# Kernel optimization log

Measured on AMD Instinct MI355X. Metric: run time of the kernel, lower is better.

Reference implementation:

```python
import jax, jax.numpy as jnp
import numpy as np

B = 262144
IN = 256
HID = 128
OUT = 15
C = 15  # num_cameras


def setup_inputs() -> dict:
    key = jax.random.key(0)
    k_x, k_c, k_w1, k_b1, k_w2, k_b2 = jax.random.split(key, 6)
    x = jax.random.normal(k_x, (B, IN), dtype=jnp.float32)
    cam = jax.random.randint(k_c, (B,), 0, C)
    # per-camera 2-layer MLP params (Linear->ReLU->Dropout(eval)->Linear)
    W1 = jax.random.normal(k_w1, (C, IN, HID), dtype=jnp.float32) / np.sqrt(IN)
    b1 = jax.random.normal(k_b1, (C, HID), dtype=jnp.float32) * 0.01
    W2 = jax.random.normal(k_w2, (C, HID, OUT), dtype=jnp.float32) / np.sqrt(HID)
    b2 = jax.random.normal(k_b2, (C, OUT), dtype=jnp.float32) * 0.01
    return {"input": x, "cam": cam, "W1": W1, "b1": b1, "W2": W2, "b2": b2}


def reference(input, cam, W1, b1, W2, b2):
    # Per-sample camera-id dispatch to one of C small MLPs, vectorized:
    # run each camera's MLP on the full batch (C is small/fixed) and select
    # each sample's output by its camera id. Dropout is identity (eval mode).
    out = jnp.zeros((input.shape[0], OUT), dtype=input.dtype)
    for c in range(C):
        h = jax.nn.relu(input @ W1[c] + b1[c])      # [B, HID]
        logits = h @ W2[c] + b2[c]                  # [B, OUT]
        out = jnp.where((cam == c)[:, None], logits, out)
    return out
```

## Files before the change

kernel.cpp:

```cpp
#include <hip/hip_runtime.h>
#include <hip/hip_bf16.h>

#define BB    262144
#define INF   256
#define HIDF  128
#define OUTF  15
#define NCAM  15
#define TM    128
#define MAXTILES (BB/TM + NCAM)

typedef __attribute__((ext_vector_type(8))) short          bf16x8;
typedef __attribute__((ext_vector_type(4))) float          floatx4;
typedef __attribute__((ext_vector_type(4))) int            intx4;
typedef __attribute__((ext_vector_type(4))) unsigned int   uintx4;
typedef __attribute__((ext_vector_type(8))) unsigned short ushortx8;

__device__ __forceinline__ unsigned short f2bf1(float a){
  unsigned int u = __builtin_bit_cast(unsigned int, a);
  u += 0x7fffu + ((u >> 16) & 1u);
  return (unsigned short)(u >> 16);
}
__device__ __forceinline__ unsigned int f2bf2(float a, float b){
  return (unsigned int)f2bf1(a) | ((unsigned int)f2bf1(b) << 16);
}

__global__ void k_prephist(const float* __restrict__ W1, const float* __restrict__ W2,
                           const int* __restrict__ cam,
                           unsigned short* __restrict__ W1p, unsigned short* __restrict__ W2p,
                           int* __restrict__ counts){
  int bid = blockIdx.x, tid = threadIdx.x;
  if (bid < 240){
    int t = bid * 256 + tid;
    int l  = t & 63;
    int kf = (t >> 6) & 7;
    int nf = (t >> 9) & 7;
    int c  = t >> 12;
    int col = nf*16 + (l & 15);
    int k0  = kf*32 + (l >> 4)*8;
    ushortx8 v;
    #pragma unroll
    for (int j = 0; j < 8; ++j)
      v[j] = f2bf1(W1[((size_t)c*INF + k0 + j)*HIDF + col]);
    *reinterpret_cast<ushortx8*>(W1p + (size_t)t*8) = v;
  } else if (bid < 255){
    int c  = bid - 240;
    int l  = tid & 63;
    int kf = tid >> 6;
    int col = l & 15;
    int k0  = kf*32 + (l >> 4)*8;
    ushortx8 v;
    #pragma unroll
    for (int j = 0; j < 8; ++j){
      float f = (col < OUTF) ? W2[((size_t)c*HIDF + k0 + j)*OUTF + col] : 0.0f;
      v[j] = f2bf1(f);
    }
    *reinterpret_cast<ushortx8*>(W2p + ((size_t)(c*4 + kf)*64 + l)*8) = v;
  } else if (bid >= 256){
    __shared__ int lc[NCAM];
    if (tid < NCAM) lc[tid] = 0;
    __syncthreads();
    intx4 v = *reinterpret_cast<const intx4*>(cam + (size_t)((bid-256)*256 + tid)*4);
    atomicAdd(&lc[v[0]], 1); atomicAdd(&lc[v[1]], 1);
    atomicAdd(&lc[v[2]], 1); atomicAdd(&lc[v[3]], 1);
    __syncthreads();
    if (tid < NCAM && lc[tid]) atomicAdd(&counts[tid], lc[tid]);
  }
}

__global__ void k_scatter(const int* __restrict__ cam, const int* __restrict__ counts,
                          int* __restrict__ scatterOfs, int* __restrict__ idx){
  __shared__ int lc[NCAM];
  __shared__ int loff[NCAM];
  __shared__ int base[NCAM];
  int t = threadIdx.x;
  if (t < NCAM) lc[t] = 0;
  __syncthreads();
  int start = blockIdx.x * 4096;
  int camr[16], lpos[16];
  #pragma unroll
  for (int j = 0; j < 16; ++j){
    int i = start + j*256 + t;
    camr[j] = cam[i];
    lpos[j] = atomicAdd(&lc[camr[j]], 1);
  }
  __syncthreads();
  if (t == 0){
    int s = 0;
    #pragma unroll
    for (int c = 0; c < NCAM; ++c){ loff[c] = s; s += counts[c]; }
  }
  __syncthreads();
  if (t < NCAM) base[t] = loff[t] + atomicAdd(&scatterOfs[t], lc[t]);
  __syncthreads();
  #pragma unroll
  for (int j = 0; j < 16; ++j)
    idx[base[camr[j]] + lpos[j]] = start + j*256 + t;
}

__global__ __launch_bounds__(256, 2) void k_mlp(
    const float* __restrict__ x, const int* __restrict__ idx,
    const int* __restrict__ counts,
    const unsigned short* __restrict__ W1p, const unsigned short* __restrict__ W2p,
    const float* __restrict__ b1, const float* __restrict__ b2,
    float* __restrict__ out)
{
  __shared__ __align__(16) char smem[65536];

  int bid = blockIdx.x;
  intx4 q0 = *reinterpret_cast<const intx4*>(counts);
  intx4 q1 = *reinterpret_cast<const intx4*>(counts + 4);
  intx4 q2 = *reinterpret_cast<const intx4*>(counts + 8);
  intx4 q3 = *reinterpret_cast<const intx4*>(counts + 12);
  int cnt[16] = {q0[0],q0[1],q0[2],q0[3], q1[0],q1[1],q1[2],q1[3],
                 q2[0],q2[1],q2[2],q2[3], q3[0],q3[1],q3[2],q3[3]};
  int c = -1, segStart = 0, rowStart = 0, rows = 0;
  {
    int cum = 0, rcum = 0;
    #pragma unroll
    for (int cc = 0; cc < NCAM; ++cc){
      int n  = cnt[cc];
      int nt = (n + TM - 1) >> 7;
      if (c < 0 && bid < cum + nt){
        c = cc;
        rowStart = (bid - cum) * TM;
        segStart = rcum;
        rows = n - rowStart; if (rows > TM) rows = TM;
      }
      cum += nt; rcum += n;
    }
  }
  if (c < 0) return;

  int t = threadIdx.x;
  int wave = t >> 6, lane = t & 63;
  int wr  = wave * 32, l15 = lane & 15, lk = lane >> 4;
  const int* idxBase = idx + segStart + rowStart;

  const char* srcp[4];
  {
    int sr = lane >> 3, su = lane & 7;
    int woff = (su ^ sr) * 16;
    #pragma unroll
    for (int i = 0; i < 4; ++i){
      int row = wr + i*8 + sr;
      int rc = (row < rows) ? row : (rows - 1);
      srcp[i] = reinterpret_cast<const char*>(x) + (size_t)idxBase[rc]*1024 + woff;
    }
  }

  const unsigned short* bbase = W1p + (size_t)c*32768 + lane*8;

#define STAGE(qq) { \
    char* db = smem + ((qq)&3)*16384 + wave*4096; \
    _Pragma("unroll") \
    for (int i = 0; i < 4; ++i){ \
      __builtin_amdgcn_global_load_lds( \
        (const __attribute__((address_space(1))) unsigned int*)(srcp[i] + (qq)*128), \
        (__attribute__((address_space(3))) unsigned int*)(db + i*1024), \
        16, 0, 0); \
    } }

  floatx4 acc[2][8];
  #pragma unroll
  for (int i = 0; i < 2; ++i)
    #pragma unroll
    for (int j = 0; j < 8; ++j) acc[i][j] = (floatx4)0.0f;

  bf16x8 bfr[2][8];
  #pragma unroll
  for (int nf = 0; nf < 8; ++nf)
    bfr[0][nf] = *reinterpret_cast<const bf16x8*>(bbase + nf*4096);
  __builtin_amdgcn_sched_barrier(0);
  STAGE(0); STAGE(1); STAGE(2);
  __builtin_amdgcn_sched_barrier(0);

  int swz8 = l15 & 7;

  #pragma unroll
  for (int kf = 0; kf < 8; ++kf){
    if (kf < 7){
      #pragma unroll
      for (int nf = 0; nf < 8; ++nf)
        bfr[(kf+1)&1][nf] = *reinterpret_cast<const bf16x8*>(bbase + nf*4096 + (kf+1)*512);
    }
    __builtin_amdgcn_sched_barrier(0);
    if (kf < 5) STAGE(kf+3);
    __builtin_amdgcn_sched_barrier(0);
    if (kf == 0)      asm volatile("s_waitcnt vmcnt(20)" ::: "memory");
    else if (kf <= 4) asm volatile("s_waitcnt vmcnt(16)" ::: "memory");
    else if (kf == 5) asm volatile("s_waitcnt vmcnt(12)" ::: "memory");
    else if (kf == 6) asm volatile("s_waitcnt vmcnt(8)"  ::: "memory");
    else              asm volatile("s_waitcnt vmcnt(0)"  ::: "memory");
    __builtin_amdgcn_sched_barrier(0);

    bf16x8 af[2];
    #pragma unroll
    for (int mf = 0; mf < 2; ++mf){
      int rl = mf*16 + l15;
      const char* rb = smem + (kf&3)*16384 + wave*4096 + rl*128;
      floatx4 f0 = *reinterpret_cast<const floatx4*>(rb + (((2*lk)   ^ swz8) * 16));
      floatx4 f1 = *reinterpret_cast<const floatx4*>(rb + (((2*lk+1) ^ swz8) * 16));
      uintx4 u;
      u[0] = f2bf2(f0[0], f0[1]); u[1] = f2bf2(f0[2], f0[3]);
      u[2] = f2bf2(f1[0], f1[1]); u[3] = f2bf2(f1[2], f1[3]);
      af[mf] = __builtin_bit_cast(bf16x8, u);
    }
    #pragma unroll
    for (int nf = 0; nf < 8; ++nf)
      acc[0][nf] = __builtin_amdgcn_mfma_f32_16x16x32_bf16(af[0], bfr[kf&1][nf], acc[0][nf], 0, 0, 0);
    #pragma unroll
    for (int nf = 0; nf < 8; ++nf)
      acc[1][nf] = __builtin_amdgcn_mfma_f32_16x16x32_bf16(af[1], bfr[kf&1][nf], acc[1][nf], 0, 0, 0);
  }

  #pragma unroll
  for (int nf = 0; nf < 8; ++nf){
    int col = nf*16 + l15;
    float bias = b1[c*HIDF + col];
    #pragma unroll
    for (int mf = 0; mf < 2; ++mf){
      #pragma unroll
      for (int j = 0; j < 4; ++j){
        int rl = mf*16 + lk*4 + j;
        float h = fmaxf(acc[mf][nf][j] + bias, 0.0f);
        int off = (rl>>4)*16384 + wave*4096 + (rl&15)*256 + ((col*2) ^ ((rl&7)<<4));
        *reinterpret_cast<unsigned short*>(smem + off) = f2bf1(h);
      }
    }
  }

  floatx4 acc2[2];
  acc2[0] = (floatx4)0.0f; acc2[1] = (floatx4)0.0f;
  const unsigned short* wb = W2p + (size_t)c*2048 + lane*8;
  #pragma unroll
  for (int kf = 0; kf < 4; ++kf){
    bf16x8 wv = *reinterpret_cast<const bf16x8*>(wb + kf*512);
    #pragma unroll
    for (int mf = 0; mf < 2; ++mf){
      int rl = mf*16 + l15;
      int off = (rl>>4)*16384 + wave*4096 + (rl&15)*256 + ((kf*64 + lk*16) ^ ((rl&7)<<4));
      bf16x8 av = *reinterpret_cast<const bf16x8*>(smem + off);
      acc2[mf] = __builtin_amdgcn_mfma_f32_16x16x32_bf16(av, wv, acc2[mf], 0, 0, 0);
    }
  }

  int col = l15;
  if (col < OUTF){
    float bias2 = b2[c*OUTF + col];
    #pragma unroll
    for (int mf = 0; mf < 2; ++mf){
      #pragma unroll
      for (int j = 0; j < 4; ++j){
        int r = wr + mf*16 + lk*4 + j;
        if (r < rows)
          out[(size_t)idxBase[r]*OUTF + col] = acc2[mf][j] + bias2;
      }
    }
  }
#undef STAGE
}

extern "C" void kernel_launch(void* const* d_in, const int* in_sizes, int n_in,
                              void* d_out, int out_size, void* d_ws, size_t ws_size,
                              hipStream_t stream) {
  const float* x  = (const float*)d_in[0];
  const int*   cam= (const int*)d_in[1];
  const float* W1 = (const float*)d_in[2];
  const float* b1 = (const float*)d_in[3];
  const float* W2 = (const float*)d_in[4];
  const float* b2 = (const float*)d_in[5];
  float* out = (float*)d_out;

  char* ws = (char*)d_ws;
  int* counts     = (int*)(ws);
  int* scatterOfs = (int*)(ws + 64);
  int* idx        = (int*)(ws + 256);
  unsigned short* W1p = (unsigned short*)(ws + 256 + (size_t)BB*4);
  unsigned short* W2p = W1p + (size_t)NCAM*8*8*64*8;

  (void)hipMemsetAsync(counts, 0, 128, stream);
  hipLaunchKernelGGL(k_prephist, dim3(512),     dim3(256), 0, stream, W1, W2, cam, W1p, W2p, counts);
  hipLaunchKernelGGL(k_scatter,  dim3(BB/4096), dim3(256), 0, stream, cam, counts, scatterOfs, idx);
  hipLaunchKernelGGL(k_mlp,      dim3(MAXTILES),dim3(256), 0, stream,
                     x, idx, counts, W1p, W2p, b1, b2, out);
}
```

Before: 93.49 us.

## Load gathered rows through registers, convert to bf16 once, stage bf16 in LDS

Replaces the 4-stage async global_load_lds pipeline of fp32 x tiles with register loads. Each wave gathers its 32 rows by shuffling row indices, converts them to bf16 with the packed v_cvt_pk_bf16_f32 instruction, and writes the full 32x256 bf16 tile into a swizzled per-wave LDS region before the MFMA loop. This removes the repeated fp32-to-bf16 conversion inside the K loop and halves the LDS footprint for A. The cost is that load/compute overlap across K steps is lost, and register pressure rises from holding 16 float4 staging values.

```diff
diff --git a/kernel.cpp b/kernel.cpp
--- a/kernel.cpp
+++ b/kernel.cpp
@@ -12,7 +12,7 @@
 typedef __attribute__((ext_vector_type(8))) short          bf16x8;
 typedef __attribute__((ext_vector_type(4))) float          floatx4;
 typedef __attribute__((ext_vector_type(4))) int            intx4;
-typedef __attribute__((ext_vector_type(4))) unsigned int   uintx4;
+typedef __attribute__((ext_vector_type(2))) unsigned int   uintx2;
 typedef __attribute__((ext_vector_type(8))) unsigned short ushortx8;
 
 __device__ __forceinline__ unsigned short f2bf1(float a){
@@ -20,8 +20,10 @@
   u += 0x7fffu + ((u >> 16) & 1u);
   return (unsigned short)(u >> 16);
 }
-__device__ __forceinline__ unsigned int f2bf2(float a, float b){
-  return (unsigned int)f2bf1(a) | ((unsigned int)f2bf1(b) << 16);
+__device__ __forceinline__ unsigned int cvtpk(float a, float b){
+  unsigned int r;
+  asm("v_cvt_pk_bf16_f32 %0, %1, %2" : "=v"(r) : "v"(a), "v"(b));
+  return r;
 }
 
 __global__ void k_prephist(const float* __restrict__ W1, const float* __restrict__ W2,
@@ -133,48 +135,54 @@
 
   int t = threadIdx.x;
   int wave = t >> 6, lane = t & 63;
-  int wr  = wave * 32, l15 = lane & 15, lk = lane >> 4;
+  int wr = wave * 32, l15 = lane & 15, lk = lane >> 4;
   const int* idxBase = idx + segStart + rowStart;
 
-  const char* srcp[4];
-  {
-    int sr = lane >> 3, su = lane & 7;
-    int woff = (su ^ sr) * 16;
-    #pragma unroll
-    for (int i = 0; i < 4; ++i){
-      int row = wr + i*8 + sr;
-      int rc = (row < rows) ? row : (rows - 1);
-      srcp[i] = reinterpret_cast<const char*>(x) + (size_t)idxBase[rc]*1024 + woff;
-    }
-  }
+  int rr = wr + (lane & 31);
+  int gl = idxBase[(rr < rows) ? rr : (rows - 1)];
+
+  char* Aw = smem + wave*16384;
+
+  floatx4 lv0[8], lv1[8];
+
+  auto LOADB = [&](int b, floatx4 (&d)[8]){
+    #pragma unroll
+    for (int i = 0; i < 8; ++i){
+      int g = __shfl(gl, b*8 + i);
+      d[i] = *reinterpret_cast<const floatx4*>(x + (size_t)g*INF + lane*4);
+    }
+  };
+  auto WRITEB = [&](int b, floatx4 (&d)[8]){
+    #pragma unroll
+    for (int i = 0; i < 8; ++i){
+      int rl = b*8 + i;
+      uintx2 u;
+      u[0] = cvtpk(d[i][0], d[i][1]);
+      u[1] = cvtpk(d[i][2], d[i][3]);
+      *reinterpret_cast<uintx2*>(Aw + rl*512 + ((lane*8) ^ ((rl & 7) << 4))) = u;
+    }
+  };
+
+  floatx4 acc[2][8];
+  #pragma unroll
+  for (int i = 0; i < 2; ++i)
+    #pragma unroll
+    for (int j = 0; j < 8; ++j) acc[i][j] = (floatx4)0.0f;
 
   const unsigned short* bbase = W1p + (size_t)c*32768 + lane*8;
-
-#define STAGE(qq) { \
-    char* db = smem + ((qq)&3)*16384 + wave*4096; \
-    _Pragma("unroll") \
-    for (int i = 0; i < 4; ++i){ \
-      __builtin_amdgcn_global_load_lds( \
-        (const __attribute__((address_space(1))) unsigned int*)(srcp[i] + (qq)*128), \
-        (__attribute__((address_space(3))) unsigned int*)(db + i*1024), \
-        16, 0, 0); \
-    } }
-
-  floatx4 acc[2][8];
-  #pragma unroll
-  for (int i = 0; i < 2; ++i)
-    #pragma unroll
-    for (int j = 0; j < 8; ++j) acc[i][j] = (floatx4)0.0f;
-
   bf16x8 bfr[2][8];
+
+  LOADB(0, lv0);
+  LOADB(1, lv1);
+  WRITEB(0, lv0);
+  LOADB(2, lv0);
+  WRITEB(1, lv1);
+  LOADB(3, lv1);
   #pragma unroll
   for (int nf = 0; nf < 8; ++nf)
     bfr[0][nf] = *reinterpret_cast<const bf16x8*>(bbase + nf*4096);
-  __builtin_amdgcn_sched_barrier(0);
-  STAGE(0); STAGE(1); STAGE(2);
-  __builtin_amdgcn_sched_barrier(0);
-
-  int swz8 = l15 & 7;
+  WRITEB(2, lv0);
+  WRITEB(3, lv1);
 
   #pragma unroll
   for (int kf = 0; kf < 8; ++kf){
@@ -183,27 +191,12 @@
       for (int nf = 0; nf < 8; ++nf)
         bfr[(kf+1)&1][nf] = *reinterpret_cast<const bf16x8*>(bbase + nf*4096 + (kf+1)*512);
     }
-    __builtin_amdgcn_sched_barrier(0);
-    if (kf < 5) STAGE(kf+3);
-    __builtin_amdgcn_sched_barrier(0);
-    if (kf == 0)      asm volatile("s_waitcnt vmcnt(20)" ::: "memory");
-    else if (kf <= 4) asm volatile("s_waitcnt vmcnt(16)" ::: "memory");
-    else if (kf == 5) asm volatile("s_waitcnt vmcnt(12)" ::: "memory");
-    else if (kf == 6) asm volatile("s_waitcnt vmcnt(8)"  ::: "memory");
-    else              asm volatile("s_waitcnt vmcnt(0)"  ::: "memory");
-    __builtin_amdgcn_sched_barrier(0);
-
     bf16x8 af[2];
     #pragma unroll
     for (int mf = 0; mf < 2; ++mf){
       int rl = mf*16 + l15;
-      const char* rb = smem + (kf&3)*16384 + wave*4096 + rl*128;
-      floatx4 f0 = *reinterpret_cast<const floatx4*>(rb + (((2*lk)   ^ swz8) * 16));
-      floatx4 f1 = *reinterpret_cast<const floatx4*>(rb + (((2*lk+1) ^ swz8) * 16));
-      uintx4 u;
-      u[0] = f2bf2(f0[0], f0[1]); u[1] = f2bf2(f0[2], f0[3]);
-      u[2] = f2bf2(f1[0], f1[1]); u[3] = f2bf2(f1[2], f1[3]);
-      af[mf] = __builtin_bit_cast(bf16x8, u);
+      af[mf] = *reinterpret_cast<const bf16x8*>(
+          Aw + rl*512 + (((kf*64 + lk*16)) ^ ((rl & 7) << 4)));
     }
     #pragma unroll
     for (int nf = 0; nf < 8; ++nf)
@@ -223,8 +216,8 @@
       for (int j = 0; j < 4; ++j){
         int rl = mf*16 + lk*4 + j;
         float h = fmaxf(acc[mf][nf][j] + bias, 0.0f);
-        int off = (rl>>4)*16384 + wave*4096 + (rl&15)*256 + ((col*2) ^ ((rl&7)<<4));
-        *reinterpret_cast<unsigned short*>(smem + off) = f2bf1(h);
+        *reinterpret_cast<unsigned short*>(
+            Aw + rl*256 + ((col*2) ^ ((rl & 7) << 4))) = f2bf1(h);
       }
     }
   }
@@ -238,8 +231,8 @@
     #pragma unroll
     for (int mf = 0; mf < 2; ++mf){
       int rl = mf*16 + l15;
-      int off = (rl>>4)*16384 + wave*4096 + (rl&15)*256 + ((kf*64 + lk*16) ^ ((rl&7)<<4));
-      bf16x8 av = *reinterpret_cast<const bf16x8*>(smem + off);
+      bf16x8 av = *reinterpret_cast<const bf16x8*>(
+          Aw + rl*256 + ((kf*64 + lk*16) ^ ((rl & 7) << 4)));
       acc2[mf] = __builtin_amdgcn_mfma_f32_16x16x32_bf16(av, wv, acc2[mf], 0, 0, 0);
     }
   }
@@ -257,7 +250,6 @@
       }
     }
   }
-#undef STAGE
 }
 
 extern "C" void kernel_launch(void* const* d_in, const int* in_sizes, int n_in,
```

New measurement: 98.95 us. 5.8% more time.

## Replace global atomic histogram with per-block counts and scan; interleave camera tiles

Applied to the files above, without the earlier changes.

Each histogram block now writes its per-camera counts to its own slot instead of atomically adding into a global array. A single-block scan kernel then computes deterministic per-block scatter offsets, which removes the memset and the atomic offset claims in the scatter kernel. The MLP grid is changed to a fixed 15×160 layout where block id mod 15 selects the camera, so tiles of different cameras run interleaved. This adds a serial scan kernel launch, and it assumes no camera has more than 160 tiles of rows.

```diff
diff --git a/kernel.cpp b/kernel.cpp
--- a/kernel.cpp
+++ b/kernel.cpp
@@ -7,7 +7,8 @@
 #define OUTF  15
 #define NCAM  15
 #define TM    128
-#define MAXTILES (BB/TM + NCAM)
+#define NSB   64
+#define PHMAX 160
 
 typedef __attribute__((ext_vector_type(8))) short          bf16x8;
 typedef __attribute__((ext_vector_type(4))) float          floatx4;
@@ -27,7 +28,7 @@
 __global__ void k_prephist(const float* __restrict__ W1, const float* __restrict__ W2,
                            const int* __restrict__ cam,
                            unsigned short* __restrict__ W1p, unsigned short* __restrict__ W2p,
-                           int* __restrict__ counts){
+                           int* __restrict__ counts2){
   int bid = blockIdx.x, tid = threadIdx.x;
   if (bid < 240){
     int t = bid * 256 + tid;
@@ -56,24 +57,52 @@
     }
     *reinterpret_cast<ushortx8*>(W2p + ((size_t)(c*4 + kf)*64 + l)*8) = v;
   } else if (bid >= 256){
-    __shared__ int lc[NCAM];
-    if (tid < NCAM) lc[tid] = 0;
+    int sb = bid - 256;
+    __shared__ int lc[16];
+    if (tid < 16) lc[tid] = 0;
     __syncthreads();
-    intx4 v = *reinterpret_cast<const intx4*>(cam + (size_t)((bid-256)*256 + tid)*4);
-    atomicAdd(&lc[v[0]], 1); atomicAdd(&lc[v[1]], 1);
-    atomicAdd(&lc[v[2]], 1); atomicAdd(&lc[v[3]], 1);
+    #pragma unroll
+    for (int i = 0; i < 4; ++i){
+      intx4 v = *reinterpret_cast<const intx4*>(cam + (size_t)sb*4096 + i*1024 + tid*4);
+      atomicAdd(&lc[v[0]], 1); atomicAdd(&lc[v[1]], 1);
+      atomicAdd(&lc[v[2]], 1); atomicAdd(&lc[v[3]], 1);
+    }
     __syncthreads();
-    if (tid < NCAM && lc[tid]) atomicAdd(&counts[tid], lc[tid]);
-  }
-}
-
-__global__ void k_scatter(const int* __restrict__ cam, const int* __restrict__ counts,
-                          int* __restrict__ scatterOfs, int* __restrict__ idx){
-  __shared__ int lc[NCAM];
-  __shared__ int loff[NCAM];
-  __shared__ int base[NCAM];
+    if (tid < 16) counts2[sb*16 + tid] = lc[tid];
+  }
+}
+
+__global__ void k_scan(const int* __restrict__ counts2, int* __restrict__ off2,
+                       int* __restrict__ counts){
+  __shared__ int tots[16];
+  int c = threadIdx.x;
+  if (c < 16){
+    int tot = 0;
+    #pragma unroll 1
+    for (int sb = 0; sb < NSB; ++sb) tot += counts2[sb*16 + c];
+    tots[c] = tot;
+    counts[c] = tot;
+  }
+  __syncthreads();
+  if (c < 16){
+    int base = 0;
+    #pragma unroll
+    for (int cc = 0; cc < 16; ++cc) if (cc < c) base += tots[cc];
+    int run = base;
+    #pragma unroll 1
+    for (int sb = 0; sb < NSB; ++sb){
+      off2[sb*16 + c] = run;
+      run += counts2[sb*16 + c];
+    }
+  }
+}
+
+__global__ void k_scatter(const int* __restrict__ cam, const int* __restrict__ off2,
+                          int* __restrict__ idx){
+  __shared__ int lc[16];
+  __shared__ int base[16];
   int t = threadIdx.x;
-  if (t < NCAM) lc[t] = 0;
+  if (t < 16) lc[t] = 0;
   __syncthreads();
   int start = blockIdx.x * 4096;
   int camr[16], lpos[16];
@@ -84,13 +113,7 @@
     lpos[j] = atomicAdd(&lc[camr[j]], 1);
   }
   __syncthreads();
-  if (t == 0){
-    int s = 0;
-    #pragma unroll
-    for (int c = 0; c < NCAM; ++c){ loff[c] = s; s += counts[c]; }
-  }
-  __syncthreads();
-  if (t < NCAM) base[t] = loff[t] + atomicAdd(&scatterOfs[t], lc[t]);
+  if (t < 16) base[t] = off2[blockIdx.x*16 + t];
   __syncthreads();
   #pragma unroll
   for (int j = 0; j < 16; ++j)
@@ -107,29 +130,22 @@
   __shared__ __align__(16) char smem[65536];
 
   int bid = blockIdx.x;
+  int c = bid % NCAM, phase = bid / NCAM;
   intx4 q0 = *reinterpret_cast<const intx4*>(counts);
   intx4 q1 = *reinterpret_cast<const intx4*>(counts + 4);
   intx4 q2 = *reinterpret_cast<const intx4*>(counts + 8);
   intx4 q3 = *reinterpret_cast<const intx4*>(counts + 12);
   int cnt[16] = {q0[0],q0[1],q0[2],q0[3], q1[0],q1[1],q1[2],q1[3],
                  q2[0],q2[1],q2[2],q2[3], q3[0],q3[1],q3[2],q3[3]};
-  int c = -1, segStart = 0, rowStart = 0, rows = 0;
-  {
-    int cum = 0, rcum = 0;
-    #pragma unroll
-    for (int cc = 0; cc < NCAM; ++cc){
-      int n  = cnt[cc];
-      int nt = (n + TM - 1) >> 7;
-      if (c < 0 && bid < cum + nt){
-        c = cc;
-        rowStart = (bid - cum) * TM;
-        segStart = rcum;
-        rows = n - rowStart; if (rows > TM) rows = TM;
-      }
-      cum += nt; rcum += n;
-    }
-  }
-  if (c < 0) return;
+  int segStart = 0, myCnt = 0;
+  #pragma unroll
+  for (int cc = 0; cc < NCAM; ++cc){
+    if (cc < c) segStart += cnt[cc];
+    if (cc == c) myCnt = cnt[cc];
+  }
+  int rowStart = phase * TM;
+  if (rowStart >= myCnt) return;
+  int rows = myCnt - rowStart; if (rows > TM) rows = TM;
 
   int t = threadIdx.x;
   int wave = t >> 6, lane = t & 63;
@@ -272,15 +288,16 @@
   float* out = (float*)d_out;
 
   char* ws = (char*)d_ws;
-  int* counts     = (int*)(ws);
-  int* scatterOfs = (int*)(ws + 64);
-  int* idx        = (int*)(ws + 256);
-  unsigned short* W1p = (unsigned short*)(ws + 256 + (size_t)BB*4);
+  int* counts  = (int*)(ws);
+  int* counts2 = (int*)(ws + 1024);
+  int* off2    = (int*)(ws + 5120);
+  int* idx     = (int*)(ws + 16384);
+  unsigned short* W1p = (unsigned short*)(ws + 16384 + (size_t)BB*4);
   unsigned short* W2p = W1p + (size_t)NCAM*8*8*64*8;
 
-  (void)hipMemsetAsync(counts, 0, 128, stream);
-  hipLaunchKernelGGL(k_prephist, dim3(512),     dim3(256), 0, stream, W1, W2, cam, W1p, W2p, counts);
-  hipLaunchKernelGGL(k_scatter,  dim3(BB/4096), dim3(256), 0, stream, cam, counts, scatterOfs, idx);
-  hipLaunchKernelGGL(k_mlp,      dim3(MAXTILES),dim3(256), 0, stream,
+  hipLaunchKernelGGL(k_prephist, dim3(320),        dim3(256), 0, stream, W1, W2, cam, W1p, W2p, counts2);
+  hipLaunchKernelGGL(k_scan,     dim3(1),          dim3(64),  0, stream, counts2, off2, counts);
+  hipLaunchKernelGGL(k_scatter,  dim3(NSB),        dim3(256), 0, stream, cam, off2, idx);
+  hipLaunchKernelGGL(k_mlp,      dim3(NCAM*PHMAX), dim3(256), 0, stream,
                      x, idx, counts, W1p, W2p, b1, b2, out);
 }
```

New measurement: 98.10 us. +4.9%, slower.
